# Kernel tuning notes

Hardware: AMD Instinct MI355X
Metric: run time of the kernel (lower is better)

The kernel has to match this reference:

```python
import jax, jax.numpy as jnp
import numpy as np

C_IN = 256
RED = 8
C_QK = C_IN // RED  # 32


def setup_inputs() -> dict:
    key = jax.random.key(0)
    ks = jax.random.split(key, 7)
    B, C, H, W = 4, C_IN, 64, 64
    s = 1.0 / np.sqrt(C)
    return {
        "x": jax.random.normal(ks[0], (B, C, H, W), dtype=jnp.float32),
        "wq": jax.random.uniform(ks[1], (C_QK, C), jnp.float32, -s, s),
        "bq": jax.random.uniform(ks[2], (C_QK,), jnp.float32, -s, s),
        "wk": jax.random.uniform(ks[3], (C_QK, C), jnp.float32, -s, s),
        "bk": jax.random.uniform(ks[4], (C_QK,), jnp.float32, -s, s),
        "wv": jax.random.uniform(ks[5], (C, C), jnp.float32, -s, s),
        "bv": jax.random.uniform(ks[6], (C,), jnp.float32, -s, s),
        "gamma": jnp.zeros((1,), dtype=jnp.float32),
    }


def reference(x, wq, bq, wk, bk, wv, bv, gamma):
    B, C, H, W = x.shape
    N = H * W
    xf = x.reshape(B, C, N)  # flatten spatial tokens
    # 1x1 convs == per-pixel linear projections over channels
    q = jnp.einsum("oc,bcn->bno", wq, xf) + bq            # (B, N, C_qk)
    k = jnp.einsum("oc,bcn->bon", wk, xf) + bk[:, None]   # (B, C_qk, N)
    v = jnp.einsum("oc,bcn->bon", wv, xf) + bv[:, None]   # (B, C, N)
    # unscaled attention: softmax over keys (last dim)
    attn = jax.nn.softmax(jnp.einsum("bio,boj->bij", q, k), axis=-1)  # (B, N, N)
    # attended[b,c,i] = sum_j v[b,c,j] * attn[b,i,j]  (bmm with attn^T)
    attended = jnp.einsum("bcj,bij->bci", v, attn).reshape(B, C, H, W)
    output = gamma[0] * attended + x
    attention_map = attn.mean(axis=1).reshape(B, H, W)
    return output, attention_map
```

## Files before the change

kernel.cpp:

```cpp
#include <hip/hip_runtime.h>


#define B_   4
#define C_   256
#define N_   4096
#define CQK_ 32
#define BCN_ (B_*C_*N_)
#define BN_  (B_*N_)

typedef __attribute__((ext_vector_type(8))) short short8v;
typedef __attribute__((ext_vector_type(4))) float f32x4;
typedef unsigned short ushort_t;

__device__ __forceinline__ ushort_t f2bf(float f) {
  unsigned u = __builtin_bit_cast(unsigned, f);
  u += 0x7FFFu + ((u >> 16) & 1u);
  return (ushort_t)(u >> 16);
}
__device__ __forceinline__ float bf2f(ushort_t h) {
  unsigned u = ((unsigned)h) << 16;
  return __builtin_bit_cast(float, u);
}

__global__ __launch_bounds__(256) void
k_prep(const float* __restrict__ x,
       const float* __restrict__ wq, const float* __restrict__ bq,
       const float* __restrict__ wk, const float* __restrict__ bk,
       const float* __restrict__ wv,
       float* __restrict__ out, float* __restrict__ l,
       ushort_t* __restrict__ wb, float* __restrict__ bqk,
       ushort_t* __restrict__ wvb, ushort_t* __restrict__ xbt) {
  __shared__ ushort_t tile[64 * 65];
  int blk = blockIdx.x, tid = threadIdx.x;
  int b = blk >> 8, cg = (blk >> 6) & 3, ng = blk & 63;
  int c0 = cg << 6, n0 = ng << 6;
  const float* xb = x + ((size_t)b * C_ + c0) * N_ + n0;
  float* ob = out + ((size_t)b * C_ + c0) * N_ + n0;
  for (int flat = tid; flat < 4096; flat += 256) {
    int r = flat >> 6, col = flat & 63;
    float v = xb[(size_t)r * N_ + col];
    ob[(size_t)r * N_ + col] = v;
    tile[r * 65 + col] = f2bf(v);
  }
  __syncthreads();
  for (int flat = tid; flat < 4096; flat += 256) {
    int nr = flat >> 6, cc = flat & 63;
    xbt[((size_t)(b * N_) + n0 + nr) * C_ + c0 + cc] = tile[cc * 65 + nr];
  }
  if (blk < 64) {
    int idx = blk * 256 + tid;
    l[idx] = 0.0f;
    out[BCN_ + idx] = 0.0f;
    wb[idx] = f2bf(idx < 8192 ? wq[idx] : wk[idx - 8192]);
    if (blk == 0 && tid < 64) bqk[tid] = tid < 32 ? bq[tid] : bk[tid - 32];
    for (int i = idx; i < 65536; i += 16384) wvb[i] = f2bf(wv[i]);
  }
}

__global__ __launch_bounds__(256) void
k_projqk(const ushort_t* __restrict__ xbt, const ushort_t* __restrict__ wb,
         const float* __restrict__ bqk,
         ushort_t* __restrict__ qb, ushort_t* __restrict__ kb) {
  int blk = blockIdx.x;
  int b = blk >> 6, ng = blk & 63;
  int wave = threadIdx.x >> 6, lane = threadIdx.x & 63;
  int col16 = lane & 15, quad = lane >> 4;
  int mt = wave;
  short8v afr[8];
#pragma unroll
  for (int ks = 0; ks < 8; ++ks)
    afr[ks] = *(const short8v*)(wb + (mt * 16 + col16) * C_ + ks * 32 + quad * 8);
  float bias[4];
#pragma unroll
  for (int r = 0; r < 4; ++r) bias[r] = bqk[mt * 16 + quad * 4 + r];
  const ushort_t* xrow = xbt + (size_t)b * N_ * C_;
  ushort_t* dst = (mt < 2) ? qb : kb;
  int co_base = (mt & 1) * 16 + quad * 4;
  for (int nt = 0; nt < 4; ++nt) {
    int n = ng * 64 + nt * 16 + col16;
    f32x4 c = {0.f, 0.f, 0.f, 0.f};
#pragma unroll
    for (int ks = 0; ks < 8; ++ks) {
      short8v bfr = *(const short8v*)(xrow + (size_t)n * C_ + ks * 32 + quad * 8);
      c = __builtin_amdgcn_mfma_f32_16x16x32_bf16(afr[ks], bfr, c, 0, 0, 0);
    }
    ushort4 pk;
    pk.x = f2bf(c[0] + bias[0]); pk.y = f2bf(c[1] + bias[1]);
    pk.z = f2bf(c[2] + bias[2]); pk.w = f2bf(c[3] + bias[3]);
    *(ushort4*)(dst + ((size_t)(b * N_) + n) * CQK_ + co_base) = pk;
  }
}

__global__ __launch_bounds__(256) void
k_projv(const ushort_t* __restrict__ xbt, const ushort_t* __restrict__ wvb,
        const float* __restrict__ bv, const float* __restrict__ gamma,
        float* __restrict__ v_t) {
  if (gamma[0] == 0.0f) return;
  int blk = blockIdx.x;
  int b = blk >> 6, ng = blk & 63;
  int wave = threadIdx.x >> 6, lane = threadIdx.x & 63;
  int col16 = lane & 15, quad = lane >> 4;
  const ushort_t* xrow = xbt + (size_t)b * N_ * C_;
  for (int nt = 0; nt < 4; ++nt) {
    int n = ng * 64 + nt * 16 + col16;
    short8v bfr[8];
#pragma unroll
    for (int ks = 0; ks < 8; ++ks)
      bfr[ks] = *(const short8v*)(xrow + (size_t)n * C_ + ks * 32 + quad * 8);
    for (int mt = wave * 4; mt < wave * 4 + 4; ++mt) {
      f32x4 c = {0.f, 0.f, 0.f, 0.f};
#pragma unroll
      for (int ks = 0; ks < 8; ++ks) {
        short8v afr = *(const short8v*)(wvb + (mt * 16 + col16) * C_ + ks * 32 + quad * 8);
        c = __builtin_amdgcn_mfma_f32_16x16x32_bf16(afr, bfr[ks], c, 0, 0, 0);
      }
      int co = mt * 16 + quad * 4;
      float4 o;
      o.x = c[0] + bv[co]; o.y = c[1] + bv[co + 1];
      o.z = c[2] + bv[co + 2]; o.w = c[3] + bv[co + 3];
      *(float4*)(v_t + ((size_t)(b * N_) + n) * C_ + co) = o;
    }
  }
}

__global__ __launch_bounds__(256) void
k_rowsA(const ushort_t* __restrict__ qb, const ushort_t* __restrict__ kb,
        float* __restrict__ l) {
  int blk = blockIdx.x;
  int b = blk >> 8, rg = (blk >> 2) & 63, js = blk & 3;
  int wave = threadIdx.x >> 6, lane = threadIdx.x & 63;
  int col16 = lane & 15, quad = lane >> 4;
  const ushort_t* qbb = qb + (size_t)b * N_ * CQK_;
  const ushort_t* kbb = kb + (size_t)b * N_ * CQK_;
  int i_base = rg * 64;
  short8v a[4];
#pragma unroll
  for (int t = 0; t < 4; ++t)
    a[t] = *(const short8v*)(qbb + (i_base + t * 16 + col16) * CQK_ + quad * 8);
  float racc[16];
#pragma unroll
  for (int r = 0; r < 16; ++r) racc[r] = 0.0f;
  int j_base = js * 1024 + wave * 256;
  for (int t = 0; t < 16; ++t) {
    short8v bfr = *(const short8v*)(kbb + (j_base + t * 16 + col16) * CQK_ + quad * 8);
#pragma unroll
    for (int m = 0; m < 4; ++m) {
      f32x4 c = {0.f, 0.f, 0.f, 0.f};
      c = __builtin_amdgcn_mfma_f32_16x16x32_bf16(a[m], bfr, c, 0, 0, 0);
      racc[m * 4 + 0] += __expf(c[0]); racc[m * 4 + 1] += __expf(c[1]);
      racc[m * 4 + 2] += __expf(c[2]); racc[m * 4 + 3] += __expf(c[3]);
    }
  }
#pragma unroll
  for (int r = 0; r < 16; ++r) {
    float v = racc[r];
    v += __shfl_xor(v, 1); v += __shfl_xor(v, 2);
    v += __shfl_xor(v, 4); v += __shfl_xor(v, 8);
    racc[r] = v;
  }
  if (col16 == 0) {
    float* lb = l + b * N_ + i_base;
#pragma unroll
    for (int m = 0; m < 4; ++m)
#pragma unroll
      for (int rr = 0; rr < 4; ++rr)
        atomicAdd(&lb[m * 16 + quad * 4 + rr], racc[m * 4 + rr]);
  }
}

__global__ __launch_bounds__(256) void
k_mapB(const ushort_t* __restrict__ qb, const ushort_t* __restrict__ kb,
       const float* __restrict__ l, float* __restrict__ map) {
  int blk = blockIdx.x;
  int b = blk >> 8, jg = (blk >> 4) & 15, isp = blk & 15;
  int wave = threadIdx.x >> 6, lane = threadIdx.x & 63;
  int col16 = lane & 15, quad = lane >> 4;
  const ushort_t* qbb = qb + (size_t)b * N_ * CQK_;
  const ushort_t* kbb = kb + (size_t)b * N_ * CQK_;
  int j_base = jg * 256 + wave * 64;
  short8v a[4];
#pragma unroll
  for (int t = 0; t < 4; ++t)
    a[t] = *(const short8v*)(kbb + (j_base + t * 16 + col16) * CQK_ + quad * 8);
  float csum[16];
#pragma unroll
  for (int r = 0; r < 16; ++r) csum[r] = 0.0f;
  int i_base = isp * 256;
  for (int t = 0; t < 16; ++t) {
    int i0 = i_base + t * 16;
    short8v bfr = *(const short8v*)(qbb + (i0 + col16) * CQK_ + quad * 8);
    float winv = 1.0f / l[b * N_ + i0 + col16];
#pragma unroll
    for (int m = 0; m < 4; ++m) {
      f32x4 c = {0.f, 0.f, 0.f, 0.f};
      c = __builtin_amdgcn_mfma_f32_16x16x32_bf16(a[m], bfr, c, 0, 0, 0);
      csum[m * 4 + 0] += __expf(c[0]) * winv; csum[m * 4 + 1] += __expf(c[1]) * winv;
      csum[m * 4 + 2] += __expf(c[2]) * winv; csum[m * 4 + 3] += __expf(c[3]) * winv;
    }
  }
#pragma unroll
  for (int r = 0; r < 16; ++r) {
    float v = csum[r];
    v += __shfl_xor(v, 1); v += __shfl_xor(v, 2);
    v += __shfl_xor(v, 4); v += __shfl_xor(v, 8);
    csum[r] = v;
  }
  if (col16 == 0) {
    float* mp = map + b * N_ + j_base;
#pragma unroll
    for (int m = 0; m < 4; ++m)
#pragma unroll
      for (int rr = 0; rr < 4; ++rr)
        atomicAdd(&mp[m * 16 + quad * 4 + rr], csum[m * 4 + rr] * (1.0f / (float)N_));
  }
}

__global__ __launch_bounds__(256) void
k_pv(const ushort_t* __restrict__ qb, const ushort_t* __restrict__ kb,
     const float* __restrict__ v_t, const float* __restrict__ l,
     const float* __restrict__ gamma, float* __restrict__ out) {
  if (gamma[0] == 0.0f) return;
  __shared__ float qs[32 * CQK_];
  __shared__ float invl[32];
  __shared__ float ps[32 * 256];
  int blk = blockIdx.x;
  int b = blk >> 9, i0 = ((blk >> 2) & 127) << 5, jsp = blk & 3;
  int tid = threadIdx.x;
  for (int r = tid; r < 32 * CQK_; r += 256)
    qs[r] = bf2f(qb[((size_t)(b * N_) + i0) * CQK_ + r]);
  if (tid < 32) invl[tid] = 1.0f / l[b * N_ + i0 + tid];
  __syncthreads();
  float g = gamma[0];
  float acc[32];
#pragma unroll
  for (int i = 0; i < 32; ++i) acc[i] = 0.0f;
  for (int jt = jsp * 4; jt < jsp * 4 + 4; ++jt) {
    int j = jt * 256 + tid;
    const ushort_t* krow = kb + ((size_t)(b * N_) + j) * CQK_;
    float kcol[CQK_];
#pragma unroll
    for (int o = 0; o < CQK_; ++o) kcol[o] = bf2f(krow[o]);
#pragma unroll
    for (int i = 0; i < 32; ++i) {
      float s = 0.0f;
#pragma unroll
      for (int o = 0; o < CQK_; ++o) s += qs[i * CQK_ + o] * kcol[o];
      ps[i * 256 + tid] = __expf(s) * invl[i];
    }
    __syncthreads();
    const float* vtb = v_t + ((size_t)(b * N_) + jt * 256) * C_;
    for (int jj = 0; jj < 256; ++jj) {
      float vv = vtb[(size_t)jj * C_ + tid];
#pragma unroll
      for (int i = 0; i < 32; ++i) acc[i] += ps[i * 256 + jj] * vv;
    }
    __syncthreads();
  }
  float* ob = out + ((size_t)(b * C_) + tid) * N_ + i0;
#pragma unroll
  for (int i = 0; i < 32; ++i) atomicAdd(&ob[i], g * acc[i]);
}

extern "C" void kernel_launch(void* const* d_in, const int* in_sizes, int n_in,
                              void* d_out, int out_size, void* d_ws, size_t ws_size,
                              hipStream_t stream) {
  const float* x     = (const float*)d_in[0];
  const float* wq    = (const float*)d_in[1];
  const float* bq    = (const float*)d_in[2];
  const float* wk    = (const float*)d_in[3];
  const float* bk    = (const float*)d_in[4];
  const float* wv    = (const float*)d_in[5];
  const float* bv    = (const float*)d_in[6];
  const float* gamma = (const float*)d_in[7];
  float* out = (float*)d_out;
  float* wsf = (float*)d_ws;
  float*    l    = wsf;
  float*    bqk  = wsf + 16384;
  ushort_t* wb   = (ushort_t*)(wsf + 16448);
  ushort_t* wvb  = (ushort_t*)(wsf + 24640);
  ushort_t* xbt  = (ushort_t*)(wsf + 57408);
  ushort_t* qb   = (ushort_t*)(wsf + 2154560);
  ushort_t* kb   = (ushort_t*)(wsf + 2416704);
  float*    v_t  = wsf + 2678848;

  k_prep  <<<1024, 256, 0, stream>>>(x, wq, bq, wk, bk, wv, out, l, wb, bqk, wvb, xbt);
  k_projqk<<< 256, 256, 0, stream>>>(xbt, wb, bqk, qb, kb);
  k_projv <<< 256, 256, 0, stream>>>(xbt, wvb, bv, gamma, v_t);
  k_rowsA <<<1024, 256, 0, stream>>>(qb, kb, l);
  k_mapB  <<<1024, 256, 0, stream>>>(qb, kb, l, out + BCN_);
  k_pv    <<<2048, 256, 0, stream>>>(qb, kb, v_t, l, gamma, out);
}
```

Measured before the change: 128.6 us.

## Fuse QK and V projections, convert weights inline, vectorize prep transpose

```diff
diff --git a/kernel.cpp b/kernel.cpp
--- a/kernel.cpp
+++ b/kernel.cpp
@@ -7,6 +7,7 @@
 #define CQK_ 32
 #define BCN_ (B_*C_*N_)
 #define BN_  (B_*N_)
+#define TP_  68
 
 typedef __attribute__((ext_vector_type(8))) short short8v;
 typedef __attribute__((ext_vector_type(4))) float f32x4;
@@ -21,103 +22,103 @@
   unsigned u = ((unsigned)h) << 16;
   return __builtin_bit_cast(float, u);
 }
-
-__global__ __launch_bounds__(256) void
-k_prep(const float* __restrict__ x,
-       const float* __restrict__ wq, const float* __restrict__ bq,
-       const float* __restrict__ wk, const float* __restrict__ bk,
-       const float* __restrict__ wv,
-       float* __restrict__ out, float* __restrict__ l,
-       ushort_t* __restrict__ wb, float* __restrict__ bqk,
-       ushort_t* __restrict__ wvb, ushort_t* __restrict__ xbt) {
-  __shared__ ushort_t tile[64 * 65];
+__device__ __forceinline__ short8v ld8f(const float* p) {
+  float4 a = *(const float4*)p, b = *(const float4*)(p + 4);
+  short8v r;
+  r[0]=f2bf(a.x); r[1]=f2bf(a.y); r[2]=f2bf(a.z); r[3]=f2bf(a.w);
+  r[4]=f2bf(b.x); r[5]=f2bf(b.y); r[6]=f2bf(b.z); r[7]=f2bf(b.w);
+  return r;
+}
+
+__global__ __launch_bounds__(256) void
+k_prep(const float* __restrict__ x, float* __restrict__ out,
+       float* __restrict__ l, ushort_t* __restrict__ xbt) {
+  __shared__ ushort_t tile[64 * TP_];
   int blk = blockIdx.x, tid = threadIdx.x;
   int b = blk >> 8, cg = (blk >> 6) & 3, ng = blk & 63;
   int c0 = cg << 6, n0 = ng << 6;
   const float* xb = x + ((size_t)b * C_ + c0) * N_ + n0;
   float* ob = out + ((size_t)b * C_ + c0) * N_ + n0;
-  for (int flat = tid; flat < 4096; flat += 256) {
-    int r = flat >> 6, col = flat & 63;
-    float v = xb[(size_t)r * N_ + col];
-    ob[(size_t)r * N_ + col] = v;
-    tile[r * 65 + col] = f2bf(v);
+#pragma unroll
+  for (int it = 0; it < 4; ++it) {
+    int flat4 = it * 256 + tid;
+    int r = flat4 >> 4, c4 = flat4 & 15;
+    float4 v = *(const float4*)(xb + (size_t)r * N_ + c4 * 4);
+    *(float4*)(ob + (size_t)r * N_ + c4 * 4) = v;
+    ushort4 h;
+    h.x = f2bf(v.x); h.y = f2bf(v.y); h.z = f2bf(v.z); h.w = f2bf(v.w);
+    *(ushort4*)(&tile[r * TP_ + c4 * 4]) = h;
   }
   __syncthreads();
-  for (int flat = tid; flat < 4096; flat += 256) {
-    int nr = flat >> 6, cc = flat & 63;
-    xbt[((size_t)(b * N_) + n0 + nr) * C_ + c0 + cc] = tile[cc * 65 + nr];
+#pragma unroll
+  for (int it = 0; it < 4; ++it) {
+    int flat4 = it * 256 + tid;
+    int nr = flat4 >> 4, cc4 = flat4 & 15;
+    ushort4 h;
+    h.x = tile[(cc4 * 4 + 0) * TP_ + nr];
+    h.y = tile[(cc4 * 4 + 1) * TP_ + nr];
+    h.z = tile[(cc4 * 4 + 2) * TP_ + nr];
+    h.w = tile[(cc4 * 4 + 3) * TP_ + nr];
+    *(ushort4*)(xbt + ((size_t)(b * N_) + n0 + nr) * C_ + c0 + cc4 * 4) = h;
   }
   if (blk < 64) {
     int idx = blk * 256 + tid;
     l[idx] = 0.0f;
     out[BCN_ + idx] = 0.0f;
-    wb[idx] = f2bf(idx < 8192 ? wq[idx] : wk[idx - 8192]);
-    if (blk == 0 && tid < 64) bqk[tid] = tid < 32 ? bq[tid] : bk[tid - 32];
-    for (int i = idx; i < 65536; i += 16384) wvb[i] = f2bf(wv[i]);
-  }
-}
-
-__global__ __launch_bounds__(256) void
-k_projqk(const ushort_t* __restrict__ xbt, const ushort_t* __restrict__ wb,
-         const float* __restrict__ bqk,
-         ushort_t* __restrict__ qb, ushort_t* __restrict__ kb) {
-  int blk = blockIdx.x;
-  int b = blk >> 6, ng = blk & 63;
+  }
+}
+
+__global__ __launch_bounds__(256) void
+k_projqk(const ushort_t* __restrict__ xbt,
+         const float* __restrict__ wq, const float* __restrict__ bq,
+         const float* __restrict__ wk, const float* __restrict__ bk,
+         const float* __restrict__ wv, const float* __restrict__ bv,
+         const float* __restrict__ gamma,
+         ushort_t* __restrict__ qb, ushort_t* __restrict__ kb,
+         float* __restrict__ v_t) {
+  int blk = blockIdx.x;
+  int b = blk >> 8, ng = blk & 255;
   int wave = threadIdx.x >> 6, lane = threadIdx.x & 63;
   int col16 = lane & 15, quad = lane >> 4;
   int mt = wave;
-  short8v afr[8];
+  bool isq = mt < 2;
+  int co_row = (mt & 1) * 16 + col16;
+  const float* wrow = (isq ? wq : wk) + co_row * C_;
+  int n = ng * 16 + col16;
+  const ushort_t* xrow = xbt + ((size_t)(b * N_) + n) * C_;
+
+  short8v bfr[8];
 #pragma unroll
   for (int ks = 0; ks < 8; ++ks)
-    afr[ks] = *(const short8v*)(wb + (mt * 16 + col16) * C_ + ks * 32 + quad * 8);
-  float bias[4];
-#pragma unroll
-  for (int r = 0; r < 4; ++r) bias[r] = bqk[mt * 16 + quad * 4 + r];
-  const ushort_t* xrow = xbt + (size_t)b * N_ * C_;
-  ushort_t* dst = (mt < 2) ? qb : kb;
+    bfr[ks] = *(const short8v*)(xrow + ks * 32 + quad * 8);
+
+  f32x4 c = {0.f, 0.f, 0.f, 0.f};
+#pragma unroll
+  for (int ks = 0; ks < 8; ++ks) {
+    short8v afr = ld8f(wrow + ks * 32 + quad * 8);
+    c = __builtin_amdgcn_mfma_f32_16x16x32_bf16(afr, bfr[ks], c, 0, 0, 0);
+  }
   int co_base = (mt & 1) * 16 + quad * 4;
-  for (int nt = 0; nt < 4; ++nt) {
-    int n = ng * 64 + nt * 16 + col16;
-    f32x4 c = {0.f, 0.f, 0.f, 0.f};
-#pragma unroll
-    for (int ks = 0; ks < 8; ++ks) {
-      short8v bfr = *(const short8v*)(xrow + (size_t)n * C_ + ks * 32 + quad * 8);
-      c = __builtin_amdgcn_mfma_f32_16x16x32_bf16(afr[ks], bfr, c, 0, 0, 0);
-    }
-    ushort4 pk;
-    pk.x = f2bf(c[0] + bias[0]); pk.y = f2bf(c[1] + bias[1]);
-    pk.z = f2bf(c[2] + bias[2]); pk.w = f2bf(c[3] + bias[3]);
-    *(ushort4*)(dst + ((size_t)(b * N_) + n) * CQK_ + co_base) = pk;
-  }
-}
-
-__global__ __launch_bounds__(256) void
-k_projv(const ushort_t* __restrict__ xbt, const ushort_t* __restrict__ wvb,
-        const float* __restrict__ bv, const float* __restrict__ gamma,
-        float* __restrict__ v_t) {
-  if (gamma[0] == 0.0f) return;
-  int blk = blockIdx.x;
-  int b = blk >> 6, ng = blk & 63;
-  int wave = threadIdx.x >> 6, lane = threadIdx.x & 63;
-  int col16 = lane & 15, quad = lane >> 4;
-  const ushort_t* xrow = xbt + (size_t)b * N_ * C_;
-  for (int nt = 0; nt < 4; ++nt) {
-    int n = ng * 64 + nt * 16 + col16;
-    short8v bfr[8];
-#pragma unroll
-    for (int ks = 0; ks < 8; ++ks)
-      bfr[ks] = *(const short8v*)(xrow + (size_t)n * C_ + ks * 32 + quad * 8);
-    for (int mt = wave * 4; mt < wave * 4 + 4; ++mt) {
-      f32x4 c = {0.f, 0.f, 0.f, 0.f};
+  const float* bias = isq ? bq : bk;
+  ushort4 pk;
+  pk.x = f2bf(c[0] + bias[co_base + 0]); pk.y = f2bf(c[1] + bias[co_base + 1]);
+  pk.z = f2bf(c[2] + bias[co_base + 2]); pk.w = f2bf(c[3] + bias[co_base + 3]);
+  ushort_t* dst = isq ? qb : kb;
+  *(ushort4*)(dst + ((size_t)(b * N_) + n) * CQK_ + co_base) = pk;
+
+  if (gamma[0] != 0.0f) {
+    for (int m2 = wave * 4; m2 < wave * 4 + 4; ++m2) {
+      f32x4 cv = {0.f, 0.f, 0.f, 0.f};
+      const float* wvr = wv + (m2 * 16 + col16) * C_;
 #pragma unroll
       for (int ks = 0; ks < 8; ++ks) {
-        short8v afr = *(const short8v*)(wvb + (mt * 16 + col16) * C_ + ks * 32 + quad * 8);
-        c = __builtin_amdgcn_mfma_f32_16x16x32_bf16(afr, bfr[ks], c, 0, 0, 0);
+        short8v afr = ld8f(wvr + ks * 32 + quad * 8);
+        cv = __builtin_amdgcn_mfma_f32_16x16x32_bf16(afr, bfr[ks], cv, 0, 0, 0);
       }
-      int co = mt * 16 + quad * 4;
+      int co = m2 * 16 + quad * 4;
       float4 o;
-      o.x = c[0] + bv[co]; o.y = c[1] + bv[co + 1];
-      o.z = c[2] + bv[co + 2]; o.w = c[3] + bv[co + 3];
+      o.x = cv[0] + bv[co];     o.y = cv[1] + bv[co + 1];
+      o.z = cv[2] + bv[co + 2]; o.w = cv[3] + bv[co + 3];
       *(float4*)(v_t + ((size_t)(b * N_) + n) * C_ + co) = o;
     }
   }
@@ -141,6 +142,7 @@
 #pragma unroll
   for (int r = 0; r < 16; ++r) racc[r] = 0.0f;
   int j_base = js * 1024 + wave * 256;
+#pragma unroll 4
   for (int t = 0; t < 16; ++t) {
     short8v bfr = *(const short8v*)(kbb + (j_base + t * 16 + col16) * CQK_ + quad * 8);
 #pragma unroll
@@ -186,6 +188,7 @@
 #pragma unroll
   for (int r = 0; r < 16; ++r) csum[r] = 0.0f;
   int i_base = isp * 256;
+#pragma unroll 4
   for (int t = 0; t < 16; ++t) {
     int i0 = i_base + t * 16;
     short8v bfr = *(const short8v*)(qbb + (i0 + col16) * CQK_ + quad * 8);
@@ -275,17 +278,13 @@
   float* out = (float*)d_out;
   float* wsf = (float*)d_ws;
   float*    l    = wsf;
-  float*    bqk  = wsf + 16384;
-  ushort_t* wb   = (ushort_t*)(wsf + 16448);
-  ushort_t* wvb  = (ushort_t*)(wsf + 24640);
-  ushort_t* xbt  = (ushort_t*)(wsf + 57408);
-  ushort_t* qb   = (ushort_t*)(wsf + 2154560);
-  ushort_t* kb   = (ushort_t*)(wsf + 2416704);
-  float*    v_t  = wsf + 2678848;
-
-  k_prep  <<<1024, 256, 0, stream>>>(x, wq, bq, wk, bk, wv, out, l, wb, bqk, wvb, xbt);
-  k_projqk<<< 256, 256, 0, stream>>>(xbt, wb, bqk, qb, kb);
-  k_projv <<< 256, 256, 0, stream>>>(xbt, wvb, bv, gamma, v_t);
+  ushort_t* xbt  = (ushort_t*)(wsf + 16384);
+  ushort_t* qb   = (ushort_t*)(wsf + 2113536);
+  ushort_t* kb   = (ushort_t*)(wsf + 2375680);
+  float*    v_t  = wsf + 2637824;
+
+  k_prep  <<<1024, 256, 0, stream>>>(x, out, l, xbt);
+  k_projqk<<<1024, 256, 0, stream>>>(xbt, wq, bq, wk, bk, wv, bv, gamma, qb, kb, v_t);
   k_rowsA <<<1024, 256, 0, stream>>>(qb, kb, l);
   k_mapB  <<<1024, 256, 0, stream>>>(qb, kb, l, out + BCN_);
   k_pv    <<<2048, 256, 0, stream>>>(qb, kb, v_t, l, gamma, out);
```

Result: slower. 133.4 us (+3.7%).
